# Kernel optimization log

Hardware: AMD Instinct MI355X
Metric: run time of the kernel (lower is better)

Reference implementation:

```python
import jax, jax.numpy as jnp
import numpy as np

KH = KW = 3  # deformable conv kernel
PAD = 1


def _bilinear_group(img, py, px):
    """img: [Cg,H,W]; py,px: [K,H,W] float sampling coords. Zero padding outside."""
    H, W = img.shape[-2], img.shape[-1]
    y0 = jnp.floor(py).astype(jnp.int32)
    x0 = jnp.floor(px).astype(jnp.int32)
    y1, x1 = y0 + 1, x0 + 1
    wy = py - y0.astype(py.dtype)
    wx = px - x0.astype(px.dtype)

    def g(yi, xi):
        yc = jnp.clip(yi, 0, H - 1)
        xc = jnp.clip(xi, 0, W - 1)
        v = img[:, yc, xc]  # [Cg,K,H,W]
        m = ((yi >= 0) & (yi < H) & (xi >= 0) & (xi < W)).astype(img.dtype)
        return v * m[None]

    return (g(y0, x0) * ((1 - wy) * (1 - wx))[None]
            + g(y0, x1) * ((1 - wy) * wx)[None]
            + g(y1, x0) * (wy * (1 - wx))[None]
            + g(y1, x1) * (wy * wx)[None])  # [Cg,K,H,W]


def reference(x, wh_pred, w_off, b_off, w_d, b_d):
    B, C, H, W = x.shape
    G = w_off.shape[0]          # deformable groups (= n_anchors)
    Cg = C // G
    K = KH * KW
    # grouped 1x1 conv: per anchor group, 2 -> 18 channels
    wh = wh_pred.reshape(B, G, 2, H, W)
    off = jnp.einsum('bgchw,goc->bgohw', wh, w_off) + b_off.reshape(G, 2 * K)[None, :, :, None, None]
    off = off.reshape(B, G, K, 2, H, W)  # channel layout: (dy, dx) per kernel tap
    # base sampling grid: p(h,w,k) = (h - PAD + kh, w - PAD + kw), stride 1
    ky, kx = jnp.meshgrid(jnp.arange(KH), jnp.arange(KW), indexing='ij')
    by = (ky.reshape(K) - PAD).astype(x.dtype)[:, None, None] + jnp.arange(H, dtype=x.dtype)[None, :, None]
    bx = (kx.reshape(K) - PAD).astype(x.dtype)[:, None, None] + jnp.arange(W, dtype=x.dtype)[None, None, :]
    py = off[:, :, :, 0] + by[None, None]  # [B,G,K,H,W]
    px = off[:, :, :, 1] + bx[None, None]
    xg = x.reshape(B, G, Cg, H, W)
    sample = jax.vmap(jax.vmap(_bilinear_group))(xg, py, px)  # [B,G,Cg,K,H,W]
    wd = w_d.reshape(w_d.shape[0], G, Cg, K)
    out = jnp.einsum('bgckhw,ogck->bohw', sample, wd) + b_d[None, :, None, None]
    return out


def setup_inputs() -> dict:
    key = jax.random.key(0)
    k = jax.random.split(key, 5)
    B, C, H, W, G = 8, 256, 64, 64, 4
    Co = 256
    return {
        'x': jax.random.normal(k[0], (B, C, H, W), jnp.float32),
        'wh_pred': jax.random.normal(k[1], (B, 2 * G, H, W), jnp.float32),
        'w_off': jax.random.normal(k[2], (G, 18, 2), jnp.float32) * 0.01,
        'b_off': jnp.zeros((2 * 9 * G,), jnp.float32),
        'w_d': jax.random.normal(k[3], (Co, C, 3, 3), jnp.float32) * (1.0 / np.sqrt(C * 9)),
        'b_d': jnp.zeros((Co,), jnp.float32),
    }
```

## Files before the change

kernel.cpp:

```cpp
#include <hip/hip_runtime.h>
#include <hip/hip_fp16.h>

typedef __attribute__((ext_vector_type(8))) _Float16 h8;
typedef __attribute__((ext_vector_type(16))) float f16v;
typedef __attribute__((ext_vector_type(4))) unsigned int u32x4;

#define NTHR 512

__device__ __forceinline__ unsigned short f2h(float f) {
    _Float16 h = (_Float16)f;
    return __builtin_bit_cast(unsigned short, h);
}
__device__ __forceinline__ __half2 u2h2(unsigned int u) {
    union { unsigned int u; __half2 h; } cv; cv.u = u; return cv.h;
}
__device__ __forceinline__ unsigned int h22u(__half2 h) {
    union { unsigned int u; __half2 h; } cv; cv.h = h; return cv.u;
}

__global__ __launch_bounds__(256) void transpose_x_kernel(
    const float* __restrict__ x, unsigned short* __restrict__ xt) {
    __shared__ float tile[64 * 65];
    const int bid = blockIdx.x;
    const int cq = bid & 3;
    const int h  = (bid >> 2) & 63;
    const int b  = bid >> 8;
    const int tid = threadIdx.x;
    const int w = tid & 63, ci = tid >> 6;
    #pragma unroll
    for (int c0 = 0; c0 < 64; c0 += 4)
        tile[(c0 + ci) * 65 + w] =
            x[(((size_t)b * 256 + cq * 64 + c0 + ci) * 64 + h) * 64 + w];
    __syncthreads();
    const int c2 = tid & 63, w2q = tid >> 6;
    #pragma unroll
    for (int w0 = 0; w0 < 64; w0 += 4) {
        int ww = w0 + w2q;
        xt[(((size_t)b * 64 + h) * 64 + ww) * 256 + cq * 64 + c2] =
            f2h(tile[c2 * 65 + ww]);
    }
}

__global__ __launch_bounds__(256) void pack_w16_kernel(const float* __restrict__ w_d,
                                                       h8* __restrict__ bp) {
    __shared__ float ldw[32 * 145];
    const int cc = blockIdx.x >> 3;
    const int nb = blockIdx.x & 7;
    const int tid = threadIdx.x;
    for (int i = tid; i < 32 * 144; i += 256) {
        int oi = i / 144, j = i - oi * 144;
        ldw[oi * 145 + j] = w_d[(size_t)(nb * 32 + oi) * 2304 + cc * 144 + j];
    }
    __syncthreads();
    for (int u = tid; u < 9 * 64; u += 256) {
        int tt = u >> 6, ll = u & 63;
        int col = ll & 31, hi2 = ll >> 5;
        h8 v;
        #pragma unroll
        for (int e = 0; e < 8; ++e)
            v[e] = (_Float16)ldw[col * 145 + (hi2 * 8 + e) * 9 + tt];
        bp[((size_t)(cc * 9 + tt) * 8 + nb) * 64 + ll] = v;
    }
}

struct PK { __half2 W00, W01, W10, W11; int A00, A01, sb; };

__global__ __launch_bounds__(NTHR, 4) void featadapt_mfma(
    const unsigned short* __restrict__ xt,
    const float* __restrict__ wh_pred,
    const float* __restrict__ w_off,
    const float* __restrict__ b_off,
    const float* __restrict__ b_d,
    const h8* __restrict__ bp,
    float* __restrict__ out)
{
    extern __shared__ unsigned char lds[];
    unsigned char* samp0 = lds;
    unsigned char* samp1 = lds + 18432;
    unsigned char* tile0 = lds + 36864;
    unsigned char* tile1 = lds + 47904;
    float* whs  = (float*)(lds + 58944);
    float* woff = (float*)(lds + 60992);
    float* boff = (float*)(lds + 61568);

    const int tid  = threadIdx.x;
    const int orig = blockIdx.x;
    const int bid  = (orig & 7) * 64 + (orig >> 3);
    const int h = bid & 63;
    const int b = bid >> 6;

    {
        int j = tid >> 6, p = tid & 63;
        whs[p * 8 + j] = wh_pred[(((size_t)b * 8 + j) * 64 + h) * 64 + p];
    }
    if (tid < 144) woff[tid] = w_off[tid];
    else if (tid < 216) boff[tid - 144] = b_off[tid - 144];

    const char* xtb = (const char*)xt + (size_t)b * (64 * 64 * 512);

    auto slotsrc = [&](int s) -> int {
        int cell = s >> 1, j = s & 1;
        int r = cell / 69, c = cell - r * 69;
        int gy = min(max(h - 2 + r, 0), 63);
        int gx = min(max(c - 2, 0), 63);
        int od = j ^ (((c >> 2) + r) & 1);
        return (gy * 64 + gx) * 512 + od * 16;
    };
    const int sg0 = slotsrc(tid);
    const int sg1 = (tid < 178) ? slotsrc(512 + tid) : 0;
    const int d0 = tid * 16, d1 = 8192 + tid * 16;

    const int l  = tid & 63;
    const int wv = tid >> 6;
    const int arow = l & 31, hi = l >> 5;
    const int ab0 = arow * 288 + hi * 16;
    const int ab1 = ab0 + 32 * 288;
    const int asw = (arow & 7) << 4;

    const int pM = wv * 8 + (l >> 3), tM = l & 7;
    const int pE = wv * 8 + (l >> 1);

    auto calcpk = [&](int p, int tap, int g, PK& S) {
        float wh0 = whs[p * 8 + 2 * g], wh1 = whs[p * 8 + 2 * g + 1];
        int oy = 2 * tap, ox = oy + 1;
        float offy = wh0 * woff[(g * 18 + oy) * 2] + wh1 * woff[(g * 18 + oy) * 2 + 1] + boff[g * 18 + oy];
        float offx = wh0 * woff[(g * 18 + ox) * 2] + wh1 * woff[(g * 18 + ox) * 2 + 1] + boff[g * 18 + ox];
        int ky = tap / 3, kx = tap - ky * 3;
        float py = offy + (float)(ky - 1 + h);
        float px = offx + (float)(kx - 1 + p);
        float fy = floorf(py), fx = floorf(px);
        int y0 = (int)fy, x0 = (int)fx;
        float wy = py - fy, wx = px - fx;
        float my0 = (y0 >= 0 && y0 < 64) ? 1.f : 0.f;
        float my1 = (y0 >= -1 && y0 < 63) ? 1.f : 0.f;
        float mx0 = (x0 >= 0 && x0 < 64) ? 1.f : 0.f;
        float mx1 = (x0 >= -1 && x0 < 63) ? 1.f : 0.f;
        S.W00 = __float2half2_rn((1.f - wy) * (1.f - wx) * my0 * mx0);
        S.W01 = __float2half2_rn((1.f - wy) * wx * my0 * mx1);
        S.W10 = __float2half2_rn(wy * (1.f - wx) * my1 * mx0);
        S.W11 = __float2half2_rn(wy * wx * my1 * mx1);
        int r0 = y0 - (h - 2);
        int c0 = x0 + 2, c1 = c0 + 1;
        S.A00 = (r0 * 69 + c0) * 32 + ((((c0 >> 2) + r0) & 1) << 4);
        S.A01 = (r0 * 69 + c1) * 32 + ((((c1 >> 2) + r0) & 1) << 4);
        S.sb  = (p * 288 + tap * 32) ^ ((p & 7) << 4);
    };

    auto sample_oct = [&](const PK& S, int oct,
                          const unsigned char* tb, unsigned char* sp) {
        int ox4 = oct << 4;
        u32x4 q00 = *(const u32x4*)(tb + (S.A00 ^ ox4));
        u32x4 q01 = *(const u32x4*)(tb + (S.A01 ^ ox4));
        u32x4 q10 = *(const u32x4*)(tb + (((S.A00 + 2208) ^ 16) ^ ox4));
        u32x4 q11 = *(const u32x4*)(tb + (((S.A01 + 2208) ^ 16) ^ ox4));
        unsigned int ow[4];
        #pragma unroll
        for (int j = 0; j < 4; ++j) {
            __half2 s = __hfma2(u2h2(q00[j]), S.W00,
                        __hfma2(u2h2(q01[j]), S.W01,
                        __hfma2(u2h2(q10[j]), S.W10,
                        __hmul2(u2h2(q11[j]), S.W11))));
            ow[j] = h22u(s);
        }
        u32x4 o4 = {ow[0], ow[1], ow[2], ow[3]};
        *(u32x4*)(sp + (S.sb ^ ox4)) = o4;
    };

    f16v acc0, acc1;
    #pragma unroll
    for (int r = 0; r < 16; ++r) { acc0[r] = 0.f; acc1[r] = 0.f; }

    {
        u32x4 t0 = *(const u32x4*)(xtb + sg0);
        u32x4 t1;
        if (tid < 178) t1 = *(const u32x4*)(xtb + sg1);
        *(u32x4*)(tile0 + d0) = t0;
        if (tid < 178) *(u32x4*)(tile0 + d1) = t1;
    }
    __syncthreads();

    PK s0, s1;
    for (int cc = 0; cc < 16; ++cc) {
        if ((cc & 3) == 0) {
            int g = cc >> 2;
            calcpk(pM, tM, g, s0);
            if (l < 16) calcpk(pE, 8, g, s1);
        }
        u32x4 n0, n1;
        if (cc < 15) {
            const int off = (cc + 1) * 32;
            n0 = *(const u32x4*)(xtb + sg0 + off);
            if (tid < 178) n1 = *(const u32x4*)(xtb + sg1 + off);
        }

        const unsigned char* tb = (cc & 1) ? tile1 : tile0;
        unsigned char* sp = (cc & 1) ? samp1 : samp0;
        sample_oct(s0, 0, tb, sp);
        sample_oct(s0, 1, tb, sp);
        if (l < 16) sample_oct(s1, l & 1, tb, sp);

        if (cc > 0) {
            const unsigned char* spp = (cc & 1) ? samp0 : samp1;
            const h8* bpc = bp + ((size_t)(cc - 1) * 9 * 8 + wv) * 64 + l;
            __builtin_amdgcn_s_setprio(1);
            #pragma unroll
            for (int tt = 0; tt < 9; ++tt) {
                h8 a0 = *(const h8*)(spp + ((ab0 + tt * 32) ^ asw));
                h8 a1 = *(const h8*)(spp + ((ab1 + tt * 32) ^ asw));
                h8 bw = bpc[(size_t)tt * 512];
                acc0 = __builtin_amdgcn_mfma_f32_32x32x16_f16(a0, bw, acc0, 0, 0, 0);
                acc1 = __builtin_amdgcn_mfma_f32_32x32x16_f16(a1, bw, acc1, 0, 0, 0);
            }
            __builtin_amdgcn_s_setprio(0);
        }

        if (cc < 15) {
            unsigned char* tn = (cc & 1) ? tile0 : tile1;
            *(u32x4*)(tn + d0) = n0;
            if (tid < 178) *(u32x4*)(tn + d1) = n1;
        }
        __syncthreads();
    }

    {
        const h8* bpc = bp + ((size_t)15 * 9 * 8 + wv) * 64 + l;
        __builtin_amdgcn_s_setprio(1);
        #pragma unroll
        for (int tt = 0; tt < 9; ++tt) {
            h8 a0 = *(const h8*)(samp1 + ((ab0 + tt * 32) ^ asw));
            h8 a1 = *(const h8*)(samp1 + ((ab1 + tt * 32) ^ asw));
            h8 bw = bpc[(size_t)tt * 512];
            acc0 = __builtin_amdgcn_mfma_f32_32x32x16_f16(a0, bw, acc0, 0, 0, 0);
            acc1 = __builtin_amdgcn_mfma_f32_32x32x16_f16(a1, bw, acc1, 0, 0, 0);
        }
        __builtin_amdgcn_s_setprio(0);
    }

    const int o = wv * 32 + arow;
    const float bd = b_d[o];
    const size_t ob = (((size_t)b * 256 + o) * 64 + h) * 64;
    #pragma unroll
    for (int q = 0; q < 4; ++q) {
        float4 s4a = make_float4(acc0[4 * q + 0] + bd, acc0[4 * q + 1] + bd,
                                 acc0[4 * q + 2] + bd, acc0[4 * q + 3] + bd);
        *(float4*)&out[ob + hi * 4 + q * 8] = s4a;
        float4 s4b = make_float4(acc1[4 * q + 0] + bd, acc1[4 * q + 1] + bd,
                                 acc1[4 * q + 2] + bd, acc1[4 * q + 3] + bd);
        *(float4*)&out[ob + 32 + hi * 4 + q * 8] = s4b;
    }
}

extern "C" void kernel_launch(void* const* d_in, const int* in_sizes, int n_in,
                              void* d_out, int out_size, void* d_ws, size_t ws_size,
                              hipStream_t stream) {
    const float* x     = (const float*)d_in[0];
    const float* whp   = (const float*)d_in[1];
    const float* w_off = (const float*)d_in[2];
    const float* b_off = (const float*)d_in[3];
    const float* w_d   = (const float*)d_in[4];
    const float* b_d   = (const float*)d_in[5];
    float* out = (float*)d_out;

    unsigned short* xt = (unsigned short*)d_ws;
    h8* bp = (h8*)((char*)d_ws + (size_t)8 * 64 * 64 * 256 * 2);

    hipLaunchKernelGGL(transpose_x_kernel, dim3(2048), dim3(256), 0, stream, x, xt);
    hipLaunchKernelGGL(pack_w16_kernel, dim3(128), dim3(256), 0, stream, w_d, bp);
    hipLaunchKernelGGL(featadapt_mfma, dim3(512), dim3(NTHR), 61856, stream,
                       xt, whp, w_off, b_off, b_d, bp, out);
}
```

Baseline: 79.79 us.

## Split each output row across two blocks of 32 pixels

```diff
diff --git a/kernel.cpp b/kernel.cpp
--- a/kernel.cpp
+++ b/kernel.cpp
@@ -76,58 +76,63 @@
 {
     extern __shared__ unsigned char lds[];
     unsigned char* samp0 = lds;
-    unsigned char* samp1 = lds + 18432;
-    unsigned char* tile0 = lds + 36864;
-    unsigned char* tile1 = lds + 47904;
-    float* whs  = (float*)(lds + 58944);
-    float* woff = (float*)(lds + 60992);
-    float* boff = (float*)(lds + 61568);
+    unsigned char* samp1 = lds + 9216;
+    unsigned char* tile0 = lds + 18432;
+    unsigned char* tile1 = lds + 24352;
+    float* whs  = (float*)(lds + 30272);
+    float* woff = (float*)(lds + 31296);
+    float* boff = (float*)(lds + 31872);
 
     const int tid  = threadIdx.x;
     const int orig = blockIdx.x;
-    const int bid  = (orig & 7) * 64 + (orig >> 3);
-    const int h = bid & 63;
-    const int b = bid >> 6;
-
-    {
-        int j = tid >> 6, p = tid & 63;
-        whs[p * 8 + j] = wh_pred[(((size_t)b * 8 + j) * 64 + h) * 64 + p];
-    }
-    if (tid < 144) woff[tid] = w_off[tid];
-    else if (tid < 216) boff[tid - 144] = b_off[tid - 144];
+    const int bid  = (orig & 7) * 128 + (orig >> 3);
+    const int mh = bid & 1;
+    const int h  = (bid >> 1) & 63;
+    const int b  = bid >> 7;
+
+    if (tid < 256) {
+        int j = tid >> 5, p = tid & 31;
+        whs[p * 8 + j] = wh_pred[(((size_t)b * 8 + j) * 64 + h) * 64 + mh * 32 + p];
+    } else if (tid < 256 + 144) {
+        woff[tid - 256] = w_off[tid - 256];
+    } else if (tid < 256 + 216) {
+        boff[tid - 400] = b_off[tid - 400];
+    }
 
     const char* xtb = (const char*)xt + (size_t)b * (64 * 64 * 512);
 
     auto slotsrc = [&](int s) -> int {
         int cell = s >> 1, j = s & 1;
-        int r = cell / 69, c = cell - r * 69;
+        int r = cell / 37, c = cell - r * 37;
         int gy = min(max(h - 2 + r, 0), 63);
-        int gx = min(max(c - 2, 0), 63);
+        int gx = min(max(mh * 32 + c - 2, 0), 63);
         int od = j ^ (((c >> 2) + r) & 1);
         return (gy * 64 + gx) * 512 + od * 16;
     };
-    const int sg0 = slotsrc(tid);
-    const int sg1 = (tid < 178) ? slotsrc(512 + tid) : 0;
-    const int d0 = tid * 16, d1 = 8192 + tid * 16;
+    const bool stg = (tid < 370);
+    const int sg0 = stg ? slotsrc(tid) : 0;
+    unsigned char* const ld0 = lds + 18432 + tid * 16;
+    const int tsel = 5920;
 
     const int l  = tid & 63;
     const int wv = tid >> 6;
     const int arow = l & 31, hi = l >> 5;
-    const int ab0 = arow * 288 + hi * 16;
-    const int ab1 = ab0 + 32 * 288;
+    const int ab  = arow * 288 + hi * 16;
     const int asw = (arow & 7) << 4;
 
-    const int pM = wv * 8 + (l >> 3), tM = l & 7;
-    const int pE = wv * 8 + (l >> 1);
-
-    auto calcpk = [&](int p, int tap, int g, PK& S) {
+    const int pkA = tid >> 1, ohA = tid & 1;
+    const bool hasB = ((tid & 7) == 0);
+    const int pkB = 256 + (tid >> 4), ohB = (tid >> 3) & 1;
+
+    auto calcpk = [&](int pk, int g, PK& S) {
+        int p = pk / 9, k = pk - p * 9;
         float wh0 = whs[p * 8 + 2 * g], wh1 = whs[p * 8 + 2 * g + 1];
-        int oy = 2 * tap, ox = oy + 1;
+        int oy = 2 * k, ox = oy + 1;
         float offy = wh0 * woff[(g * 18 + oy) * 2] + wh1 * woff[(g * 18 + oy) * 2 + 1] + boff[g * 18 + oy];
         float offx = wh0 * woff[(g * 18 + ox) * 2] + wh1 * woff[(g * 18 + ox) * 2 + 1] + boff[g * 18 + ox];
-        int ky = tap / 3, kx = tap - ky * 3;
+        int ky = k / 3, kx = k - ky * 3;
         float py = offy + (float)(ky - 1 + h);
-        float px = offx + (float)(kx - 1 + p);
+        float px = offx + (float)(kx - 1 + mh * 32 + p);
         float fy = floorf(py), fx = floorf(px);
         int y0 = (int)fy, x0 = (int)fx;
         float wy = py - fy, wx = px - fx;
@@ -140,10 +145,10 @@
         S.W10 = __float2half2_rn(wy * (1.f - wx) * my1 * mx0);
         S.W11 = __float2half2_rn(wy * wx * my1 * mx1);
         int r0 = y0 - (h - 2);
-        int c0 = x0 + 2, c1 = c0 + 1;
-        S.A00 = (r0 * 69 + c0) * 32 + ((((c0 >> 2) + r0) & 1) << 4);
-        S.A01 = (r0 * 69 + c1) * 32 + ((((c1 >> 2) + r0) & 1) << 4);
-        S.sb  = (p * 288 + tap * 32) ^ ((p & 7) << 4);
+        int c0 = x0 - mh * 32 + 2, c1 = c0 + 1;
+        S.A00 = (r0 * 37 + c0) * 32 + ((((c0 >> 2) + r0) & 1) << 4);
+        S.A01 = (r0 * 37 + c1) * 32 + ((((c1 >> 2) + r0) & 1) << 4);
+        S.sb  = (p * 288 + k * 32) ^ ((p & 7) << 4);
     };
 
     auto sample_oct = [&](const PK& S, int oct,
@@ -151,8 +156,8 @@
         int ox4 = oct << 4;
         u32x4 q00 = *(const u32x4*)(tb + (S.A00 ^ ox4));
         u32x4 q01 = *(const u32x4*)(tb + (S.A01 ^ ox4));
-        u32x4 q10 = *(const u32x4*)(tb + (((S.A00 + 2208) ^ 16) ^ ox4));
-        u32x4 q11 = *(const u32x4*)(tb + (((S.A01 + 2208) ^ 16) ^ ox4));
+        u32x4 q10 = *(const u32x4*)(tb + (((S.A00 + 1184) ^ 16) ^ ox4));
+        u32x4 q11 = *(const u32x4*)(tb + (((S.A01 + 1184) ^ 16) ^ ox4));
         unsigned int ow[4];
         #pragma unroll
         for (int j = 0; j < 4; ++j) {
@@ -166,16 +171,13 @@
         *(u32x4*)(sp + (S.sb ^ ox4)) = o4;
     };
 
-    f16v acc0, acc1;
-    #pragma unroll
-    for (int r = 0; r < 16; ++r) { acc0[r] = 0.f; acc1[r] = 0.f; }
-
-    {
+    f16v acc;
+    #pragma unroll
+    for (int r = 0; r < 16; ++r) acc[r] = 0.f;
+
+    if (stg) {
         u32x4 t0 = *(const u32x4*)(xtb + sg0);
-        u32x4 t1;
-        if (tid < 178) t1 = *(const u32x4*)(xtb + sg1);
-        *(u32x4*)(tile0 + d0) = t0;
-        if (tid < 178) *(u32x4*)(tile0 + d1) = t1;
+        *(u32x4*)ld0 = t0;
     }
     __syncthreads();
 
@@ -183,21 +185,17 @@
     for (int cc = 0; cc < 16; ++cc) {
         if ((cc & 3) == 0) {
             int g = cc >> 2;
-            calcpk(pM, tM, g, s0);
-            if (l < 16) calcpk(pE, 8, g, s1);
-        }
-        u32x4 n0, n1;
-        if (cc < 15) {
-            const int off = (cc + 1) * 32;
-            n0 = *(const u32x4*)(xtb + sg0 + off);
-            if (tid < 178) n1 = *(const u32x4*)(xtb + sg1 + off);
-        }
+            calcpk(pkA, g, s0);
+            if (hasB) calcpk(pkB, g, s1);
+        }
+        u32x4 n0;
+        if (cc < 15 && stg)
+            n0 = *(const u32x4*)(xtb + sg0 + (cc + 1) * 32);
 
         const unsigned char* tb = (cc & 1) ? tile1 : tile0;
         unsigned char* sp = (cc & 1) ? samp1 : samp0;
-        sample_oct(s0, 0, tb, sp);
-        sample_oct(s0, 1, tb, sp);
-        if (l < 16) sample_oct(s1, l & 1, tb, sp);
+        sample_oct(s0, ohA, tb, sp);
+        if (hasB) sample_oct(s1, ohB, tb, sp);
 
         if (cc > 0) {
             const unsigned char* spp = (cc & 1) ? samp0 : samp1;
@@ -205,19 +203,16 @@
             __builtin_amdgcn_s_setprio(1);
             #pragma unroll
             for (int tt = 0; tt < 9; ++tt) {
-                h8 a0 = *(const h8*)(spp + ((ab0 + tt * 32) ^ asw));
-                h8 a1 = *(const h8*)(spp + ((ab1 + tt * 32) ^ asw));
+                h8 a  = *(const h8*)(spp + ((ab + tt * 32) ^ asw));
                 h8 bw = bpc[(size_t)tt * 512];
-                acc0 = __builtin_amdgcn_mfma_f32_32x32x16_f16(a0, bw, acc0, 0, 0, 0);
-                acc1 = __builtin_amdgcn_mfma_f32_32x32x16_f16(a1, bw, acc1, 0, 0, 0);
+                acc = __builtin_amdgcn_mfma_f32_32x32x16_f16(a, bw, acc, 0, 0, 0);
             }
             __builtin_amdgcn_s_setprio(0);
         }
 
-        if (cc < 15) {
-            unsigned char* tn = (cc & 1) ? tile0 : tile1;
-            *(u32x4*)(tn + d0) = n0;
-            if (tid < 178) *(u32x4*)(tn + d1) = n1;
+        if (cc < 15 && stg) {
+            unsigned char* tn = ld0 + ((cc & 1) ? 0 : tsel);
+            *(u32x4*)tn = n0;
         }
         __syncthreads();
     }
@@ -227,26 +222,21 @@
         __builtin_amdgcn_s_setprio(1);
         #pragma unroll
         for (int tt = 0; tt < 9; ++tt) {
-            h8 a0 = *(const h8*)(samp1 + ((ab0 + tt * 32) ^ asw));
-            h8 a1 = *(const h8*)(samp1 + ((ab1 + tt * 32) ^ asw));
+            h8 a  = *(const h8*)(samp1 + ((ab + tt * 32) ^ asw));
             h8 bw = bpc[(size_t)tt * 512];
-            acc0 = __builtin_amdgcn_mfma_f32_32x32x16_f16(a0, bw, acc0, 0, 0, 0);
-            acc1 = __builtin_amdgcn_mfma_f32_32x32x16_f16(a1, bw, acc1, 0, 0, 0);
+            acc = __builtin_amdgcn_mfma_f32_32x32x16_f16(a, bw, acc, 0, 0, 0);
         }
         __builtin_amdgcn_s_setprio(0);
     }
 
     const int o = wv * 32 + arow;
     const float bd = b_d[o];
-    const size_t ob = (((size_t)b * 256 + o) * 64 + h) * 64;
+    const size_t ob = (((size_t)b * 256 + o) * 64 + h) * 64 + mh * 32;
     #pragma unroll
     for (int q = 0; q < 4; ++q) {
-        float4 s4a = make_float4(acc0[4 * q + 0] + bd, acc0[4 * q + 1] + bd,
-                                 acc0[4 * q + 2] + bd, acc0[4 * q + 3] + bd);
-        *(float4*)&out[ob + hi * 4 + q * 8] = s4a;
-        float4 s4b = make_float4(acc1[4 * q + 0] + bd, acc1[4 * q + 1] + bd,
-                                 acc1[4 * q + 2] + bd, acc1[4 * q + 3] + bd);
-        *(float4*)&out[ob + 32 + hi * 4 + q * 8] = s4b;
+        float4 s4 = make_float4(acc[4 * q + 0] + bd, acc[4 * q + 1] + bd,
+                                acc[4 * q + 2] + bd, acc[4 * q + 3] + bd);
+        *(float4*)&out[ob + hi * 4 + q * 8] = s4;
     }
 }
 
@@ -266,6 +256,6 @@
 
     hipLaunchKernelGGL(transpose_x_kernel, dim3(2048), dim3(256), 0, stream, x, xt);
     hipLaunchKernelGGL(pack_w16_kernel, dim3(128), dim3(256), 0, stream, w_d, bp);
-    hipLaunchKernelGGL(featadapt_mfma, dim3(512), dim3(NTHR), 61856, stream,
+    hipLaunchKernelGGL(featadapt_mfma, dim3(1024), dim3(NTHR), 32160, stream,
                        xt, whp, w_off, b_off, b_d, bp, out);
 }
```

Result: slower. 90.69 us (+13.7%).
